# Kernel optimization log

Hardware: AMD Instinct MI355X
Metric: run time of the kernel (lower is better)

## Reference

```python
import jax, jax.numpy as jnp
import numpy as np

D_MODEL = 1024
N_HEADS = 16


def setup_inputs() -> dict:
    key = jax.random.key(0)
    k1, k2, k3 = jax.random.split(key, 3)
    x = jax.random.normal(k1, (4, 2048, D_MODEL), dtype=jnp.float32)
    # torch nn.Linear(D, 3D): weight (3D, D), bias (3D)
    W = jax.random.normal(k2, (3 * D_MODEL, D_MODEL), dtype=jnp.float32) * (D_MODEL ** -0.5)
    b = jax.random.normal(k3, (3 * D_MODEL,), dtype=jnp.float32) * 0.01
    return {"x": x, "W": W, "b": b}


def reference(x, W, b):
    N, C, D = x.shape
    H = N_HEADS
    hd = D // H
    z = jnp.einsum("ncd,ed->nce", x, W) + b  # [N, C, 3D]
    k = z[:, :, :D].reshape(N, C, H, hd).transpose(0, 2, 1, 3)
    q = z[:, :, D:2 * D].reshape(N, C, H, hd).transpose(0, 2, 1, 3)
    v = z[:, :, 2 * D:].reshape(N, C, H, hd).transpose(0, 2, 1, 3)
    # NOTE: original scales by full model dim D, not head dim
    scores = jnp.einsum("nhqd,nhkd->nhqk", q, k) * (D ** -0.5)
    causal = jnp.tril(jnp.ones((C, C), dtype=bool))
    scores = jnp.where(causal[None, None], scores, -jnp.inf)
    attn = jax.nn.softmax(scores, axis=-1)
    out = jnp.einsum("nhqk,nhkd->nhqd", attn, v)
    return out.transpose(0, 2, 1, 3).reshape(N, C, D)
```

## Files before the change

### kernel.cpp

```cpp
#include <hip/hip_runtime.h>
#include <hip/hip_bf16.h>

typedef __bf16 bf16;
typedef __bf16 bf16x8 __attribute__((ext_vector_type(8)));
typedef float f32x4 __attribute__((ext_vector_type(4)));
typedef unsigned int u32x4 __attribute__((ext_vector_type(4)));

#define SEQ   2048
#define NBAT  4
#define DM    1024
#define NH    16
#define HD    64
#define E3    3072

__global__ void cvt2_bf16_kernel(const float* __restrict__ a, bf16* __restrict__ oa, int na8,
                                 const float* __restrict__ b, bf16* __restrict__ ob, int nb8) {
  const int stride = gridDim.x * blockDim.x;
  const int ntot = na8 + nb8;
  for (int i = blockIdx.x * blockDim.x + threadIdx.x; i < ntot; i += stride) {
    const float* src;
    bf16* dst;
    int j;
    if (i < na8) { src = a; dst = oa; j = i; }
    else         { src = b; dst = ob; j = i - na8; }
    const float4* p = (const float4*)(src + (size_t)j * 8);
    float4 x = p[0];
    float4 y = p[1];
    bf16x8 o;
    o[0] = (bf16)x.x; o[1] = (bf16)x.y; o[2] = (bf16)x.z; o[3] = (bf16)x.w;
    o[4] = (bf16)y.x; o[5] = (bf16)y.y; o[6] = (bf16)y.z; o[7] = (bf16)y.w;
    *(bf16x8*)(dst + (size_t)j * 8) = o;
  }
}

#define BM 128
#define BN 128
#define BK 32
#define KSTEPS (DM / BK)

__global__ __launch_bounds__(256, 2) void qkv_gemm_kernel(
    const bf16* __restrict__ A, const bf16* __restrict__ B,
    const float* __restrict__ bias, bf16* __restrict__ Z)
{
  __shared__ bf16 sA[2][BM * BK];
  __shared__ bf16 sB[2][BN * BK];

  const int tid  = threadIdx.x;
  const int lane = tid & 63;
  const int w    = tid >> 6;
  const int wr   = w >> 1;
  const int wc   = w & 1;
  const int m0   = blockIdx.x * BM;
  const int n0   = blockIdx.y * BN;

  const f32x4 z4 = {0.f, 0.f, 0.f, 0.f};
  f32x4 acc[4][4];
#pragma unroll
  for (int i = 0; i < 4; ++i)
#pragma unroll
    for (int j = 0; j < 4; ++j)
      acc[i][j] = z4;

  const int srow = w * 32 + (lane >> 2);
  const int skk  = (lane & 3) * 8;
  const bf16* gA = A + (size_t)m0 * DM;
  const bf16* gB = B + (size_t)n0 * DM;

  auto stage = [&](int buf, int t) {
    const int k0 = t * BK;
#pragma unroll
    for (int c = 0; c < 2; ++c)
      __builtin_amdgcn_global_load_lds(
          (const __attribute__((address_space(1))) unsigned int*)(gA + (size_t)(srow + c * 16) * DM + k0 + skk),
          (__attribute__((address_space(3))) unsigned int*)(&sA[buf][w * 1024 + c * 512]),
          16, 0, 0);
#pragma unroll
    for (int c = 0; c < 2; ++c)
      __builtin_amdgcn_global_load_lds(
          (const __attribute__((address_space(1))) unsigned int*)(gB + (size_t)(srow + c * 16) * DM + k0 + skk),
          (__attribute__((address_space(3))) unsigned int*)(&sB[buf][w * 1024 + c * 512]),
          16, 0, 0);
  };

  stage(0, 0);
  int cur = 0;
  const int arow = wr * 64 + (lane & 15);
  const int brow = wc * 64 + (lane & 15);
  const int kf   = (lane >> 4) * 8;

  for (int t = 0; t < KSTEPS; ++t) {
    __syncthreads();
    if (t + 1 < KSTEPS) stage(cur ^ 1, t + 1);
    bf16x8 af[4], bfr[4];
#pragma unroll
    for (int i = 0; i < 4; ++i)
      af[i] = *(const bf16x8*)&sA[cur][(arow + i * 16) * BK + kf];
#pragma unroll
    for (int j = 0; j < 4; ++j)
      bfr[j] = *(const bf16x8*)&sB[cur][(brow + j * 16) * BK + kf];
#pragma unroll
    for (int i = 0; i < 4; ++i)
#pragma unroll
      for (int j = 0; j < 4; ++j)
        acc[i][j] = __builtin_amdgcn_mfma_f32_16x16x32_bf16(af[i], bfr[j], acc[i][j], 0, 0, 0);
    cur ^= 1;
  }

#pragma unroll
  for (int i = 0; i < 4; ++i) {
#pragma unroll
    for (int j = 0; j < 4; ++j) {
      const int col = n0 + wc * 64 + j * 16 + (lane & 15);
      const float bb = bias[col];
#pragma unroll
      for (int r = 0; r < 4; ++r) {
        const int row = m0 + wr * 64 + i * 16 + (lane >> 4) * 4 + r;
        Z[(size_t)row * E3 + col] = (bf16)(acc[i][j][r] + bb);
      }
    }
  }
}

#define QB 64
#define KB 64
#define NQT (SEQ / QB)

__global__ __launch_bounds__(256, 4) void attn_kernel(
    const bf16* __restrict__ Z, float* __restrict__ out)
{
  __shared__ bf16 sK[2][KB][64];
  __shared__ bf16 sVT[2][HD][64];

  const int tid   = threadIdx.x;
  const int lane  = tid & 63;
  const int w     = tid >> 6;
  const int l15   = lane & 15;
  const int lhi   = lane >> 4;
  const int l7    = l15 & 7;
  const int e2    = l15 >> 3;

  const int flat = blockIdx.x + 16 * (blockIdx.y + 16 * blockIdx.z);
  const int v    = (flat & 7) * 128 + (flat >> 3);
  const int bx   = v & 15;
  const int h    = (v >> 4) & 15;
  const int n    = v >> 8;

  const size_t zb = (size_t)n * SEQ * E3;
  const int kcol0 = h * HD;
  const int qcol0 = DM + h * HD;
  const int vcol0 = 2 * DM + h * HD;

  const f32x4 z4 = {0.f, 0.f, 0.f, 0.f};
  const f32x4 neg4 = {-1e32f, -1e32f, -1e32f, -1e32f};
  const float scale = 0.03125f;
  const float L2E   = 1.4426950408889634f;
  const float SL2E  = scale * L2E;

  const u32x4 onesu = {0x3F803F80u, 0x3F803F80u, 0x3F803F80u, 0x3F803F80u};
  const bf16x8 onesf = __builtin_bit_cast(bf16x8, onesu);

  const int c0row = tid >> 3;
  const int t7    = tid & 7;
  const int c0col = t7 * 8;
  const int sgk = ((c0row & 12) << 1) | ((c0row & 16) >> 2) | (c0row & 3);

  const int krow_in = lane >> 3;
  const int kdblk   = ((lane & 7) ^ (lane >> 3)) * 8;

  const size_t ob = (size_t)n * SEQ * DM;

  bf16x8 vpre[2];
  auto vload = [&](int t) {
#pragma unroll
    for (int c = 0; c < 2; ++c)
      vpre[c] = *(const bf16x8*)&Z[zb + (size_t)(t * KB + c0row + 32 * c) * E3 + vcol0 + c0col];
  };
  auto lwriteV = [&](int buf) {
#pragma unroll
    for (int c = 0; c < 2; ++c)
#pragma unroll
      for (int j = 0; j < 8; ++j)
        sVT[buf][c0col + j][(sgk + 32 * c) ^ ((j ^ t7) << 3)] = vpre[c][j];
  };
  auto stageK = [&](int t, int buf) {
#pragma unroll
    for (int c = 0; c < 2; ++c) {
      const int cc = 2 * w + c;
      __builtin_amdgcn_global_load_lds(
          (const __attribute__((address_space(1))) unsigned int*)(
              Z + zb + (size_t)(t * KB + 8 * cc + krow_in) * E3 + kcol0 + kdblk),
          (__attribute__((address_space(3))) unsigned int*)(&sK[buf][8 * cc][0]),
          16, 0, 0);
    }
  };

#pragma unroll 1
  for (int phase = 0; phase < 2; ++phase) {
    const int qtile = phase == 0 ? bx : (NQT - 1 - bx);
    const int qwave = qtile * QB + w * 16;
    const int T     = qtile + 1;

    bf16x8 qf[2];
    {
      const int qrow = qwave + l15;
#pragma unroll
      for (int kk = 0; kk < 2; ++kk)
        qf[kk] = *(const bf16x8*)&Z[zb + (size_t)qrow * E3 + qcol0 + kk * 32 + lhi * 8];
    }

    f32x4 accO[4];
    f32x4 accL;
#pragma unroll
    for (int dt = 0; dt < 4; ++dt) accO[dt] = z4;
    accL = z4;

    stageK(0, 0);
    vload(0);
    lwriteV(0);
    if (T > 1) vload(1);
    __syncthreads();

#pragma unroll 1
    for (int t = 0; t < T; ++t) {
      const int cur = t & 1;
      if (t + 1 < T) { stageK(t + 1, cur ^ 1); lwriteV(cur ^ 1); }
      if (t + 2 < T) vload(t + 2);

      f32x4 st[4];
      __builtin_amdgcn_s_setprio(1);
#pragma unroll
      for (int kt = 0; kt < 4; ++kt) {
        const int blk0 = (lhi ^ l7) * 8;
        const int blk1 = ((4 + lhi) ^ l7) * 8;
        bf16x8 kf0 = *(const bf16x8*)&sK[cur][kt * 16 + l15][blk0];
        st[kt] = __builtin_amdgcn_mfma_f32_16x16x32_bf16(kf0, qf[0], z4, 0, 0, 0);
        bf16x8 kf1 = *(const bf16x8*)&sK[cur][kt * 16 + l15][blk1];
        st[kt] = __builtin_amdgcn_mfma_f32_16x16x32_bf16(kf1, qf[1], st[kt], 0, 0, 0);
      }
      __builtin_amdgcn_s_setprio(0);

      if (t == T - 1) {
#pragma unroll
        for (int kt = 0; kt < 4; ++kt) {
          if (kt > w) st[kt] = neg4;
          else if (kt == w) {
#pragma unroll
            for (int r = 0; r < 4; ++r)
              if (lhi * 4 + r > l15) st[kt][r] = -1e32f;
          }
        }
      }

      bf16x8 pb[2];
#pragma unroll
      for (int c = 0; c < 2; ++c) {
        u32x4 pu;
#pragma unroll
        for (int i = 0; i < 4; ++i) {
          const int kt = 2 * c + (i >> 1);
          const int r  = (2 * i) & 3;
          const float p0 = exp2f(st[kt][r]     * SL2E);
          const float p1 = exp2f(st[kt][r + 1] * SL2E);
          const bf16 b0v = (bf16)p0;
          const bf16 b1v = (bf16)p1;
          pu[i] = (unsigned int)__builtin_bit_cast(unsigned short, b0v)
                | ((unsigned int)__builtin_bit_cast(unsigned short, b1v) << 16);
        }
        pb[c] = __builtin_bit_cast(bf16x8, pu);
      }

      __builtin_amdgcn_s_setprio(1);
#pragma unroll
      for (int c = 0; c < 2; ++c)
        accL = __builtin_amdgcn_mfma_f32_16x16x32_bf16(onesf, pb[c], accL, 0, 0, 0);

#pragma unroll
      for (int c = 0; c < 2; ++c) {
#pragma unroll
        for (int dt = 0; dt < 4; ++dt) {
          const int idx = ((4 * c + lhi) ^ (l7 ^ ((2 * dt + e2) & 7))) << 3;
          const bf16x8 av = *(const bf16x8*)&sVT[cur][dt * 16 + l15][idx];
          accO[dt] = __builtin_amdgcn_mfma_f32_16x16x32_bf16(av, pb[c], accO[dt], 0, 0, 0);
        }
      }
      __builtin_amdgcn_s_setprio(0);

      __syncthreads();
    }

    {
      const float inv  = 1.f / accL[0];
      const int   qrow = qwave + l15;
#pragma unroll
      for (int dt = 0; dt < 4; ++dt) {
        float4 o;
        o.x = accO[dt][0] * inv;
        o.y = accO[dt][1] * inv;
        o.z = accO[dt][2] * inv;
        o.w = accO[dt][3] * inv;
        *(float4*)&out[ob + (size_t)qrow * DM + h * HD + dt * 16 + lhi * 4] = o;
      }
    }
  }
}

extern "C" void kernel_launch(void* const* d_in, const int* in_sizes, int n_in,
                              void* d_out, int out_size, void* d_ws, size_t ws_size,
                              hipStream_t stream) {
  const float* x    = (const float*)d_in[0];
  const float* W    = (const float*)d_in[1];
  const float* bias = (const float*)d_in[2];
  float* out = (float*)d_out;

  bf16* xb = (bf16*)d_ws;
  bf16* Wb = xb + (size_t)NBAT * SEQ * DM;
  bf16* Zb = Wb + (size_t)E3 * DM;

  cvt2_bf16_kernel<<<1536, 256, 0, stream>>>(x, xb, NBAT * SEQ * DM / 8,
                                             W, Wb, E3 * DM / 8);

  dim3 g1(NBAT * SEQ / BM, E3 / BN);
  qkv_gemm_kernel<<<g1, 256, 0, stream>>>(xb, Wb, bias, Zb);

  dim3 g2(NQT / 2, NH, NBAT);
  attn_kernel<<<g2, 256, 0, stream>>>(Zb, out);
}
```

Measured before the change: 157.5 us.

## Double attention query tile to 128 rows per block, sharing K/V tiles

Each wave now handles two 16-row query subtiles against every staged K/V tile, so each block covers 128 query rows and the K and V tiles are loaded into LDS half as often per query row. Causal masking is reworked for the wider tile, and the grid becomes a 1-D launch of 512 blocks with an XCD-aware mapping of head/batch contexts. Occupancy bounds drop from 4 to 2 blocks per CU to leave room for the doubled accumulators. Fewer blocks and coarser causal tiles may reduce parallelism and worsen load balance.

```diff
diff --git a/kernel.cpp b/kernel.cpp
--- a/kernel.cpp
+++ b/kernel.cpp
@@ -121,11 +121,11 @@
   }
 }
 
-#define QB 64
+#define QB 128
 #define KB 64
 #define NQT (SEQ / QB)
 
-__global__ __launch_bounds__(256, 4) void attn_kernel(
+__global__ __launch_bounds__(256, 2) void attn_kernel(
     const bf16* __restrict__ Z, float* __restrict__ out)
 {
   __shared__ bf16 sK[2][KB][64];
@@ -139,11 +139,13 @@
   const int l7    = l15 & 7;
   const int e2    = l15 >> 3;
 
-  const int flat = blockIdx.x + 16 * (blockIdx.y + 16 * blockIdx.z);
-  const int v    = (flat & 7) * 128 + (flat >> 3);
-  const int bx   = v & 15;
-  const int h    = (v >> 4) & 15;
-  const int n    = v >> 8;
+  const int flat  = blockIdx.x;
+  const int xcd   = flat & 7;
+  const int idx   = flat >> 3;
+  const int ctx   = xcd * 8 + (idx & 7);
+  const int pairb = idx >> 3;
+  const int h     = ctx & 15;
+  const int n     = ctx >> 4;
 
   const size_t zb = (size_t)n * SEQ * E3;
   const int kcol0 = h * HD;
@@ -196,28 +198,32 @@
 
 #pragma unroll 1
   for (int phase = 0; phase < 2; ++phase) {
-    const int qtile = phase == 0 ? bx : (NQT - 1 - bx);
-    const int qwave = qtile * QB + w * 16;
-    const int T     = qtile + 1;
-
-    bf16x8 qf[2];
-    {
-      const int qrow = qwave + l15;
+    const int qtile = phase == 0 ? pairb : (NQT - 1 - pairb);
+    const int qwave = qtile * QB + w * 32;
+    const int T     = 2 * qtile + 2;
+
+    bf16x8 qf[2][2];
+#pragma unroll
+    for (int qs = 0; qs < 2; ++qs) {
+      const int qrow = qwave + qs * 16 + l15;
 #pragma unroll
       for (int kk = 0; kk < 2; ++kk)
-        qf[kk] = *(const bf16x8*)&Z[zb + (size_t)qrow * E3 + qcol0 + kk * 32 + lhi * 8];
-    }
-
-    f32x4 accO[4];
-    f32x4 accL;
-#pragma unroll
-    for (int dt = 0; dt < 4; ++dt) accO[dt] = z4;
-    accL = z4;
+        qf[qs][kk] = *(const bf16x8*)&Z[zb + (size_t)qrow * E3 + qcol0 + kk * 32 + lhi * 8];
+    }
+
+    f32x4 accO[2][4];
+    f32x4 accL[2];
+#pragma unroll
+    for (int qs = 0; qs < 2; ++qs) {
+#pragma unroll
+      for (int dt = 0; dt < 4; ++dt) accO[qs][dt] = z4;
+      accL[qs] = z4;
+    }
 
     stageK(0, 0);
     vload(0);
     lwriteV(0);
-    if (T > 1) vload(1);
+    vload(1);
     __syncthreads();
 
 #pragma unroll 1
@@ -226,78 +232,94 @@
       if (t + 1 < T) { stageK(t + 1, cur ^ 1); lwriteV(cur ^ 1); }
       if (t + 2 < T) vload(t + 2);
 
-      f32x4 st[4];
+      f32x4 st[2][4];
       __builtin_amdgcn_s_setprio(1);
 #pragma unroll
       for (int kt = 0; kt < 4; ++kt) {
         const int blk0 = (lhi ^ l7) * 8;
         const int blk1 = ((4 + lhi) ^ l7) * 8;
         bf16x8 kf0 = *(const bf16x8*)&sK[cur][kt * 16 + l15][blk0];
-        st[kt] = __builtin_amdgcn_mfma_f32_16x16x32_bf16(kf0, qf[0], z4, 0, 0, 0);
         bf16x8 kf1 = *(const bf16x8*)&sK[cur][kt * 16 + l15][blk1];
-        st[kt] = __builtin_amdgcn_mfma_f32_16x16x32_bf16(kf1, qf[1], st[kt], 0, 0, 0);
+#pragma unroll
+        for (int qs = 0; qs < 2; ++qs) {
+          st[qs][kt] = __builtin_amdgcn_mfma_f32_16x16x32_bf16(kf0, qf[qs][0], z4, 0, 0, 0);
+          st[qs][kt] = __builtin_amdgcn_mfma_f32_16x16x32_bf16(kf1, qf[qs][1], st[qs][kt], 0, 0, 0);
+        }
       }
       __builtin_amdgcn_s_setprio(0);
 
-      if (t == T - 1) {
-#pragma unroll
-        for (int kt = 0; kt < 4; ++kt) {
-          if (kt > w) st[kt] = neg4;
-          else if (kt == w) {
-#pragma unroll
-            for (int r = 0; r < 4; ++r)
-              if (lhi * 4 + r > l15) st[kt][r] = -1e32f;
+      if (t >= 2 * qtile) {
+        const int tb = 4 * (t - 2 * qtile);
+#pragma unroll
+        for (int qs = 0; qs < 2; ++qs) {
+          const int dgq = 2 * w + qs;
+#pragma unroll
+          for (int kt = 0; kt < 4; ++kt) {
+            const int fg = tb + kt;
+            if (fg > dgq) st[qs][kt] = neg4;
+            else if (fg == dgq) {
+#pragma unroll
+              for (int r = 0; r < 4; ++r)
+                if (lhi * 4 + r > l15) st[qs][kt][r] = -1e32f;
+            }
           }
         }
       }
 
-      bf16x8 pb[2];
+      bf16x8 pb[2][2];
+#pragma unroll
+      for (int qs = 0; qs < 2; ++qs)
+#pragma unroll
+        for (int c = 0; c < 2; ++c) {
+          u32x4 pu;
+#pragma unroll
+          for (int i = 0; i < 4; ++i) {
+            const int kt = 2 * c + (i >> 1);
+            const int r  = (2 * i) & 3;
+            const float p0 = exp2f(st[qs][kt][r]     * SL2E);
+            const float p1 = exp2f(st[qs][kt][r + 1] * SL2E);
+            const bf16 b0v = (bf16)p0;
+            const bf16 b1v = (bf16)p1;
+            pu[i] = (unsigned int)__builtin_bit_cast(unsigned short, b0v)
+                  | ((unsigned int)__builtin_bit_cast(unsigned short, b1v) << 16);
+          }
+          pb[qs][c] = __builtin_bit_cast(bf16x8, pu);
+        }
+
+      __builtin_amdgcn_s_setprio(1);
+#pragma unroll
+      for (int c = 0; c < 2; ++c)
+#pragma unroll
+        for (int qs = 0; qs < 2; ++qs)
+          accL[qs] = __builtin_amdgcn_mfma_f32_16x16x32_bf16(onesf, pb[qs][c], accL[qs], 0, 0, 0);
+
 #pragma unroll
       for (int c = 0; c < 2; ++c) {
-        u32x4 pu;
-#pragma unroll
-        for (int i = 0; i < 4; ++i) {
-          const int kt = 2 * c + (i >> 1);
-          const int r  = (2 * i) & 3;
-          const float p0 = exp2f(st[kt][r]     * SL2E);
-          const float p1 = exp2f(st[kt][r + 1] * SL2E);
-          const bf16 b0v = (bf16)p0;
-          const bf16 b1v = (bf16)p1;
-          pu[i] = (unsigned int)__builtin_bit_cast(unsigned short, b0v)
-                | ((unsigned int)__builtin_bit_cast(unsigned short, b1v) << 16);
+#pragma unroll
+        for (int dt = 0; dt < 4; ++dt) {
+          const int idxv = ((4 * c + lhi) ^ (l7 ^ ((2 * dt + e2) & 7))) << 3;
+          const bf16x8 av = *(const bf16x8*)&sVT[cur][dt * 16 + l15][idxv];
+#pragma unroll
+          for (int qs = 0; qs < 2; ++qs)
+            accO[qs][dt] = __builtin_amdgcn_mfma_f32_16x16x32_bf16(av, pb[qs][c], accO[qs][dt], 0, 0, 0);
         }
-        pb[c] = __builtin_bit_cast(bf16x8, pu);
-      }
-
-      __builtin_amdgcn_s_setprio(1);
-#pragma unroll
-      for (int c = 0; c < 2; ++c)
-        accL = __builtin_amdgcn_mfma_f32_16x16x32_bf16(onesf, pb[c], accL, 0, 0, 0);
-
-#pragma unroll
-      for (int c = 0; c < 2; ++c) {
-#pragma unroll
-        for (int dt = 0; dt < 4; ++dt) {
-          const int idx = ((4 * c + lhi) ^ (l7 ^ ((2 * dt + e2) & 7))) << 3;
-          const bf16x8 av = *(const bf16x8*)&sVT[cur][dt * 16 + l15][idx];
-          accO[dt] = __builtin_amdgcn_mfma_f32_16x16x32_bf16(av, pb[c], accO[dt], 0, 0, 0);
-        }
       }
       __builtin_amdgcn_s_setprio(0);
 
       __syncthreads();
     }
 
-    {
-      const float inv  = 1.f / accL[0];
-      const int   qrow = qwave + l15;
+#pragma unroll
+    for (int qs = 0; qs < 2; ++qs) {
+      const float inv  = 1.f / accL[qs][0];
+      const int   qrow = qwave + qs * 16 + l15;
 #pragma unroll
       for (int dt = 0; dt < 4; ++dt) {
         float4 o;
-        o.x = accO[dt][0] * inv;
-        o.y = accO[dt][1] * inv;
-        o.z = accO[dt][2] * inv;
-        o.w = accO[dt][3] * inv;
+        o.x = accO[qs][dt][0] * inv;
+        o.y = accO[qs][dt][1] * inv;
+        o.z = accO[qs][dt][2] * inv;
+        o.w = accO[qs][dt][3] * inv;
         *(float4*)&out[ob + (size_t)qrow * DM + h * HD + dt * 16 + lhi * 4] = o;
       }
     }
@@ -322,6 +344,5 @@
   dim3 g1(NBAT * SEQ / BM, E3 / BN);
   qkv_gemm_kernel<<<g1, 256, 0, stream>>>(xb, Wb, bias, Zb);
 
-  dim3 g2(NQT / 2, NH, NBAT);
-  attn_kernel<<<g2, 256, 0, stream>>>(Zb, out);
+  attn_kernel<<<512, 256, 0, stream>>>(Zb, out);
 }
```

Result: no change. 158.9 us (+0.9%).
